# Kernel tuning notes

Measured on AMD Instinct MI355X. Metric: run time of the kernel, lower is better.

Reference implementation:

```python
import jax, jax.numpy as jnp
import numpy as np

B, H, L, DK = 8, 8, 256, 64
C = 5                 # num_clusters
DMODEL = H * DK       # 512, must equal d_k*h
U = 10 * C            # unfolding window = 50


def setup_inputs() -> dict:
    key = jax.random.key(0)
    ks = jax.random.split(key, 6)
    s = 0.05
    return {
        "K": jax.random.normal(ks[0], (B, H, L, DK), jnp.float32),
        "V": jax.random.normal(ks[1], (B, H, L, DK), jnp.float32),
        "W_k": jax.random.normal(ks[2], (DMODEL, C), jnp.float32) * s,
        "b_k": jnp.zeros((C,), jnp.float32),
        "W_q": jax.random.normal(ks[3], (DMODEL, C), jnp.float32) * s,
        "b_q": jnp.zeros((C,), jnp.float32),
        "W_back": jax.random.normal(ks[4], (C, DMODEL), jnp.float32) * s,
        "b_back": jnp.zeros((DMODEL,), jnp.float32),
    }


def _gelu(x):
    return jax.nn.gelu(x, approximate=False)  # torch default exact GELU


def reference(K, V, W_k, b_k, W_q, b_q, W_back, b_back):
    b, h, l_k, d_k = K.shape
    u = U
    num_c = W_k.shape[1]
    # torch: cat([zeros(u,h,l,d), K[1:]]) then unfold(0, u, 1) -> [b,h,l,d,u]
    padding = jnp.zeros((u, h, l_k, d_k), K.dtype)
    K_padded = jnp.concatenate([padding, K[1:]], axis=0)        # [u+b-1,h,l,d]
    idx = jnp.arange(b)[:, None] + jnp.arange(u)[None, :]        # [b,u]
    K_unf = jnp.moveaxis(K_padded[idx], 1, -1)                   # [b,h,l,d,u]
    # faithful row-major reshape, as in torch .reshape(b, l_k, -1, d_k*h)
    K_unf = K_unf.reshape(b, l_k, u, d_k * h)                    # [b,l,u,dm]

    cluster_k = jax.nn.softmax(_gelu(K_unf @ W_k + b_k), axis=-1)  # [b,l,u,C]
    cluster_q = jax.nn.softmax(_gelu(K_unf @ W_q + b_q), axis=-1)  # [b,l,u,C]

    mu = jnp.mean(cluster_q, axis=-1)                            # [b,l,u]
    sigma = jax.nn.softplus(jnp.std(cluster_q, axis=-1, ddof=1))  # unbiased std
    x = jnp.mean(cluster_k, axis=-1)
    log_prob = -0.5 * ((x - mu) / sigma) ** 2 - jnp.log(sigma) - 0.5 * jnp.log(2.0 * jnp.pi)
    # torch CrossEntropyLoss(mu, mu): input [N=b, C=l_k, d=u], soft prob targets
    ce = jnp.mean(jnp.sum(-mu * jax.nn.log_softmax(mu, axis=1), axis=1))
    loss = -jnp.mean(log_prob) + ce

    ind = jnp.argmax(cluster_q, axis=-1)                         # [b,l,u]
    # masked_fill_ zeroes positions whose argmax == i, then mean over u
    mask = ind[None] == jnp.arange(num_c)[:, None, None, None]   # [C,b,l,u]
    centers = jnp.mean(
        jnp.where(mask[..., None], 0.0, cluster_q[None]), axis=3
    )                                                            # [C,b,l,C]
    cc = _gelu(centers @ W_back + b_back)                        # [C,b,l,dm]
    cc = cc.reshape(b, h, num_c, l_k, d_k)                       # faithful reshape
    cc = jnp.max(cc, axis=2)                                     # [b,h,l,d]
    return cc, loss
```

## Files before the change

### kernel.cpp

```cpp
#include <hip/hip_runtime.h>
#include <math.h>

#define CC 5
#define NOUT 1048576

__device__ __forceinline__ float gelu_exact(float x) {
    return 0.5f * x * (1.0f + erff(x * 0.70710678118654752f));
}

__global__ __launch_bounds__(256) void cluster_main(
    const float* __restrict__ K,
    const float* __restrict__ Wk, const float* __restrict__ bk,
    const float* __restrict__ Wq, const float* __restrict__ bq,
    float* __restrict__ ws_mu, float* __restrict__ ws_lp, float* __restrict__ ws_ctr)
{
    const int tid  = threadIdx.x;
    const int wave = tid >> 6;
    const int lane = tid & 63;
    const int unit = wave * 512 + blockIdx.x;
    const int b    = unit >> 8;
    const int lp   = unit & 255;
    const int h    = lp >> 5;
    const int l0   = (lp & 31) << 3;

    __shared__ float4 WW4[512 * 3];
    __shared__ float  Ksh[4][3584];

    for (int m = tid; m < 512; m += 256) {
        const float* wkp = Wk + m * 5;
        const float* wqp = Wq + m * 5;
        WW4[m * 3 + 0] = make_float4(wkp[0], wkp[1], wkp[2], wkp[3]);
        WW4[m * 3 + 1] = make_float4(wkp[4], wqp[0], wqp[1], wqp[2]);
        WW4[m * 3 + 2] = make_float4(wqp[3], wqp[4], 0.f, 0.f);
    }
    __syncthreads();

    float* ksh = Ksh[wave];
    const int nk = b << 9;
    for (int i = lane; i < nk; i += 64) {
        int bp = i >> 9, sd = i & 511;
        ksh[sd * b + bp] = K[((((bp + 1) * 8 + h) * 256) + (l0 + (sd >> 6))) * 64 + (sd & 63)];
    }

    const int u = lane;
    if (u < 50) {
        float ak[CC], aq[CC];
        #pragma unroll
        for (int c = 0; c < CC; ++c) { ak[c] = bk[c]; aq[c] = bq[c]; }

        const int q0 = u << 9;
        const int r0 = q0 % 50;
        const int start = (50 - b) - r0;
        int B = q0 / 50;
        for (int st = start; st < 512; st += 50, ++B) {
            int jlo = st < 0 ? -st : 0;
            int jhi = min(b, 512 - st);
            const float* kp = ksh + B * b;
            for (int j = jlo; j < jhi; ++j) {
                float x = kp[j];
                int mm = (st + j) * 3;
                float4 w0 = WW4[mm], w1 = WW4[mm + 1], w2 = WW4[mm + 2];
                ak[0] = fmaf(x, w0.x, ak[0]);
                ak[1] = fmaf(x, w0.y, ak[1]);
                ak[2] = fmaf(x, w0.z, ak[2]);
                ak[3] = fmaf(x, w0.w, ak[3]);
                ak[4] = fmaf(x, w1.x, ak[4]);
                aq[0] = fmaf(x, w1.y, aq[0]);
                aq[1] = fmaf(x, w1.z, aq[1]);
                aq[2] = fmaf(x, w1.w, aq[2]);
                aq[3] = fmaf(x, w2.x, aq[3]);
                aq[4] = fmaf(x, w2.y, aq[4]);
            }
        }

        float gk[CC], gq[CC];
        float mk = -1e30f, mq = -1e30f;
        #pragma unroll
        for (int c = 0; c < CC; ++c) {
            gk[c] = gelu_exact(ak[c]); mk = fmaxf(mk, gk[c]);
            gq[c] = gelu_exact(aq[c]); mq = fmaxf(mq, gq[c]);
        }
        float sk = 0.f, sq = 0.f;
        #pragma unroll
        for (int c = 0; c < CC; ++c) {
            gk[c] = expf(gk[c] - mk); sk += gk[c];
            gq[c] = expf(gq[c] - mq); sq += gq[c];
        }
        float rsk = 1.f / sk, rsq = 1.f / sq;
        float qv[CC];
        float sumq = 0.f, sumk = 0.f;
        #pragma unroll
        for (int c = 0; c < CC; ++c) {
            float kvc = gk[c] * rsk; sumk += kvc;
            qv[c] = gq[c] * rsq;     sumq += qv[c];
        }
        float mu = sumq * 0.2f;
        float xb = sumk * 0.2f;
        float var = 0.f;
        #pragma unroll
        for (int c = 0; c < CC; ++c) { float dq = qv[c] - mu; var = fmaf(dq, dq, var); }
        var *= 0.25f;
        float sd_ = sqrtf(var);
        float sigma = log1pf(expf(sd_));
        float z = (xb - mu) / sigma;
        float logp = -0.5f * z * z - logf(sigma) - 0.91893853320467274f;
        int ind = 0; float bv = qv[0];
        #pragma unroll
        for (int c = 1; c < CC; ++c) if (qv[c] > bv) { bv = qv[c]; ind = c; }

        ws_mu[(b * 50 + u) * 256 + lp] = mu;

        float* row = ksh + u * 7;
        #pragma unroll
        for (int c = 0; c < CC; ++c) row[c] = qv[c];
        row[5] = (float)ind;
        row[6] = logp;
    }

    asm volatile("s_waitcnt lgkmcnt(0)" ::: "memory");

    const int t = lane;
    if (t < 26) {
        const float fi = (float)(t / 5);
        const int sel = (t < 25) ? (t % 5) : 6;
        const bool always = (t == 25);
        float acc = 0.f;
        for (int u2 = 0; u2 < 50; ++u2) {
            float v = ksh[u2 * 7 + sel];
            float f = ksh[u2 * 7 + 5];
            acc += (always || f != fi) ? v : 0.f;
        }
        if (t < 25) ws_ctr[unit * 25 + t] = acc * 0.02f;
        else        ws_lp[unit] = acc;
    }
}

__global__ __launch_bounds__(256) void backmap(
    const float* __restrict__ Wb, const float* __restrict__ bb,
    const float* __restrict__ ws_ctr, float* __restrict__ out)
{
    const int o = blockIdx.x * 256 + threadIdx.x;
    const int b2  = o >> 17;
    const int h2  = (o >> 14) & 7;
    const int r14 = o & 16383;
    const int m   = r14 & 511;
    const float w0 = Wb[m], w1 = Wb[512 + m], w2 = Wb[1024 + m], w3 = Wb[1536 + m], w4 = Wb[2048 + m];
    const float bias = bb[m];
    const int pbase = b2 * 655360 + h2 * 81920 + r14;
    float best = -INFINITY;
    #pragma unroll
    for (int c2 = 0; c2 < 5; ++c2) {
        int p = pbase + c2 * 16384;
        int c = p >> 20;
        int unit = (p & 1048575) >> 9;
        const float* ct = ws_ctr + unit * 25 + c * 5;
        float v = bias;
        v = fmaf(ct[0], w0, v);
        v = fmaf(ct[1], w1, v);
        v = fmaf(ct[2], w2, v);
        v = fmaf(ct[3], w3, v);
        v = fmaf(ct[4], w4, v);
        v = gelu_exact(v);
        best = fmaxf(best, v);
    }
    out[o] = best;
}

__global__ __launch_bounds__(1024) void finalize(
    const float* __restrict__ ws_mu, const float* __restrict__ ws_lp,
    float* __restrict__ out)
{
    const int tid  = threadIdx.x;
    const int wave = tid >> 6;
    const int lane = tid & 63;
    __shared__ float red[1024];
    __shared__ float total_lp_sh;
    __shared__ float cew[16];

    red[tid] = ws_lp[tid] + ws_lp[tid + 1024];
    __syncthreads();
    for (int s = 512; s > 0; s >>= 1) {
        if (tid < s) red[tid] += red[tid + s];
        __syncthreads();
    }
    if (tid == 0) total_lp_sh = red[0];

    float ce_part = 0.0f;
    for (int pair = wave; pair < 400; pair += 16) {
        const float* mp = ws_mu + pair * 256;
        float v0 = mp[lane], v1 = mp[lane + 64], v2 = mp[lane + 128], v3 = mp[lane + 192];
        float mx = fmaxf(fmaxf(v0, v1), fmaxf(v2, v3));
        #pragma unroll
        for (int off = 1; off < 64; off <<= 1) mx = fmaxf(mx, __shfl_xor(mx, off, 64));
        float se = expf(v0 - mx) + expf(v1 - mx) + expf(v2 - mx) + expf(v3 - mx);
        #pragma unroll
        for (int off = 1; off < 64; off <<= 1) se += __shfl_xor(se, off, 64);
        float lse = mx + logf(se);
        float a = -(v0 * (v0 - lse) + v1 * (v1 - lse) + v2 * (v2 - lse) + v3 * (v3 - lse));
        #pragma unroll
        for (int off = 1; off < 64; off <<= 1) a += __shfl_xor(a, off, 64);
        ce_part += a;
    }
    if (lane == 0) cew[wave] = ce_part;
    __syncthreads();
    if (tid == 0) {
        float ce = 0.0f;
        #pragma unroll
        for (int w = 0; w < 16; ++w) ce += cew[w];
        ce *= (1.0f / 400.0f);
        float loss = -(total_lp_sh * (1.0f / 102400.0f)) + ce;
        out[NOUT] = loss;
    }
}

extern "C" void kernel_launch(void* const* d_in, const int* in_sizes, int n_in,
                              void* d_out, int out_size, void* d_ws, size_t ws_size,
                              hipStream_t stream) {
    const float* K  = (const float*)d_in[0];
    const float* Wk = (const float*)d_in[2];
    const float* bk = (const float*)d_in[3];
    const float* Wq = (const float*)d_in[4];
    const float* bq = (const float*)d_in[5];
    const float* Wb = (const float*)d_in[6];
    const float* bb = (const float*)d_in[7];
    float* out    = (float*)d_out;
    float* ws_mu  = (float*)d_ws;
    float* ws_lp  = ws_mu + 102400;
    float* ws_ctr = ws_lp + 2048;

    cluster_main<<<512, 256, 0, stream>>>(K, Wk, bk, Wq, bq, ws_mu, ws_lp, ws_ctr);
    backmap<<<NOUT / 256, 256, 0, stream>>>(Wb, bb, ws_ctr, out);
    finalize<<<1, 1024, 0, stream>>>(ws_mu, ws_lp, out);
}
```

Baseline: 62.60 us.

## Split cluster dot products across 8 lanes per window and fuse backmap with finalize

cluster_main now runs one unit per 512-thread block, not one unit per wave. Each window position's reduction is split across 8 lanes by source batch, with the partial sums combined through shuffles. K is staged in block-shared memory with a padded layout. The back-projection stages the ten centre vectors in shared memory and uses GELU's shape to evaluate only at the min and max pre-activation. It is merged with the loss finalisation into one launch, which removes a kernel launch. The trade-offs are more blocks with lower per-thread work, extra block syncs, and reliance on GELU's max occurring at the argument extremes.

Measured after the change: 63.81 us. About the same (+1.9%).

```diff
diff --git a/kernel.cpp b/kernel.cpp
--- a/kernel.cpp
+++ b/kernel.cpp
@@ -8,57 +8,57 @@
     return 0.5f * x * (1.0f + erff(x * 0.70710678118654752f));
 }
 
-__global__ __launch_bounds__(256) void cluster_main(
+__global__ __launch_bounds__(512) void cluster_main(
     const float* __restrict__ K,
     const float* __restrict__ Wk, const float* __restrict__ bk,
     const float* __restrict__ Wq, const float* __restrict__ bq,
     float* __restrict__ ws_mu, float* __restrict__ ws_lp, float* __restrict__ ws_ctr)
 {
-    const int tid  = threadIdx.x;
-    const int wave = tid >> 6;
-    const int lane = tid & 63;
-    const int unit = wave * 512 + blockIdx.x;
+    const int blk  = blockIdx.x;
+    const int unit = ((blk & 7) << 8) | (blk >> 3);
     const int b    = unit >> 8;
     const int lp   = unit & 255;
     const int h    = lp >> 5;
     const int l0   = (lp & 31) << 3;
+    const int tid  = threadIdx.x;
 
     __shared__ float4 WW4[512 * 3];
-    __shared__ float  Ksh[4][3584];
-
-    for (int m = tid; m < 512; m += 256) {
-        const float* wkp = Wk + m * 5;
-        const float* wqp = Wq + m * 5;
-        WW4[m * 3 + 0] = make_float4(wkp[0], wkp[1], wkp[2], wkp[3]);
-        WW4[m * 3 + 1] = make_float4(wkp[4], wqp[0], wqp[1], wqp[2]);
-        WW4[m * 3 + 2] = make_float4(wqp[3], wqp[4], 0.f, 0.f);
-    }
-    __syncthreads();
-
-    float* ksh = Ksh[wave];
+    __shared__ float  ksh[7 * 516];
+    __shared__ float  rows[50 * 8];
+
+    {
+        const float* wkp = Wk + tid * 5;
+        const float* wqp = Wq + tid * 5;
+        WW4[tid * 3 + 0] = make_float4(wkp[0], wkp[1], wkp[2], wkp[3]);
+        WW4[tid * 3 + 1] = make_float4(wkp[4], wqp[0], wqp[1], wqp[2]);
+        WW4[tid * 3 + 2] = make_float4(wqp[3], wqp[4], 0.f, 0.f);
+    }
     const int nk = b << 9;
-    for (int i = lane; i < nk; i += 64) {
+    for (int i = tid; i < nk; i += 512) {
         int bp = i >> 9, sd = i & 511;
-        ksh[sd * b + bp] = K[((((bp + 1) * 8 + h) * 256) + (l0 + (sd >> 6))) * 64 + (sd & 63)];
-    }
-
-    const int u = lane;
-    if (u < 50) {
-        float ak[CC], aq[CC];
-        #pragma unroll
-        for (int c = 0; c < CC; ++c) { ak[c] = bk[c]; aq[c] = bq[c]; }
-
+        ksh[bp * 516 + sd] =
+            K[((((bp + 1) * 8 + h) * 256) + (l0 + (sd >> 6))) * 64 + (sd & 63)];
+    }
+    __syncthreads();
+
+    const int u = tid >> 3;
+    const int j = tid & 7;
+
+    float ak[CC] = {0.f, 0.f, 0.f, 0.f, 0.f};
+    float aq[CC] = {0.f, 0.f, 0.f, 0.f, 0.f};
+    if (u < 50 && j < b) {
+        const int usrc = 50 - b + j;
         const int q0 = u << 9;
         const int r0 = q0 % 50;
-        const int start = (50 - b) - r0;
-        int B = q0 / 50;
-        for (int st = start; st < 512; st += 50, ++B) {
-            int jlo = st < 0 ? -st : 0;
-            int jhi = min(b, 512 - st);
-            const float* kp = ksh + B * b;
-            for (int j = jlo; j < jhi; ++j) {
-                float x = kp[j];
-                int mm = (st + j) * 3;
+        int delta = usrc - r0; if (delta < 0) delta += 50;
+        int m = delta;
+        int B = (q0 + delta) / 50;
+        const float* kp = ksh + j * 516;
+        #pragma unroll
+        for (int it = 0; it < 11; ++it) {
+            if (m < 512) {
+                float x = kp[B];
+                int mm = m * 3;
                 float4 w0 = WW4[mm], w1 = WW4[mm + 1], w2 = WW4[mm + 2];
                 ak[0] = fmaf(x, w0.x, ak[0]);
                 ak[1] = fmaf(x, w0.y, ak[1]);
@@ -71,14 +71,25 @@
                 aq[3] = fmaf(x, w2.x, aq[3]);
                 aq[4] = fmaf(x, w2.y, aq[4]);
             }
-        }
-
+            m += 50; ++B;
+        }
+    }
+    #pragma unroll
+    for (int off = 4; off; off >>= 1) {
+        #pragma unroll
+        for (int c = 0; c < CC; ++c) {
+            ak[c] += __shfl_down(ak[c], off, 8);
+            aq[c] += __shfl_down(aq[c], off, 8);
+        }
+    }
+
+    if (u < 50 && j == 0) {
         float gk[CC], gq[CC];
         float mk = -1e30f, mq = -1e30f;
         #pragma unroll
         for (int c = 0; c < CC; ++c) {
-            gk[c] = gelu_exact(ak[c]); mk = fmaxf(mk, gk[c]);
-            gq[c] = gelu_exact(aq[c]); mq = fmaxf(mq, gq[c]);
+            gk[c] = gelu_exact(ak[c] + bk[c]); mk = fmaxf(mk, gk[c]);
+            gq[c] = gelu_exact(aq[c] + bq[c]); mq = fmaxf(mq, gq[c]);
         }
         float sk = 0.f, sq = 0.f;
         #pragma unroll
@@ -109,68 +120,73 @@
         for (int c = 1; c < CC; ++c) if (qv[c] > bv) { bv = qv[c]; ind = c; }
 
         ws_mu[(b * 50 + u) * 256 + lp] = mu;
-
-        float* row = ksh + u * 7;
+        float* row = rows + u * 8;
         #pragma unroll
         for (int c = 0; c < CC; ++c) row[c] = qv[c];
         row[5] = (float)ind;
         row[6] = logp;
     }
-
-    asm volatile("s_waitcnt lgkmcnt(0)" ::: "memory");
-
-    const int t = lane;
-    if (t < 26) {
-        const float fi = (float)(t / 5);
-        const int sel = (t < 25) ? (t % 5) : 6;
-        const bool always = (t == 25);
+    __syncthreads();
+
+    if (tid < 26) {
+        const float fi = (float)(tid / 5);
+        const int sel = (tid < 25) ? (tid % 5) : 6;
+        const bool always = (tid == 25);
         float acc = 0.f;
         for (int u2 = 0; u2 < 50; ++u2) {
-            float v = ksh[u2 * 7 + sel];
-            float f = ksh[u2 * 7 + 5];
+            float v = rows[u2 * 8 + sel];
+            float f = rows[u2 * 8 + 5];
             acc += (always || f != fi) ? v : 0.f;
         }
-        if (t < 25) ws_ctr[unit * 25 + t] = acc * 0.02f;
-        else        ws_lp[unit] = acc;
-    }
-}
-
-__global__ __launch_bounds__(256) void backmap(
+        if (tid < 25) ws_ctr[unit * 25 + tid] = acc * 0.02f;
+        else          ws_lp[unit] = acc;
+    }
+}
+
+__global__ __launch_bounds__(1024) void backfin(
     const float* __restrict__ Wb, const float* __restrict__ bb,
-    const float* __restrict__ ws_ctr, float* __restrict__ out)
+    const float* __restrict__ ws_ctr, const float* __restrict__ ws_mu,
+    const float* __restrict__ ws_lp, float* __restrict__ out)
 {
-    const int o = blockIdx.x * 256 + threadIdx.x;
-    const int b2  = o >> 17;
-    const int h2  = (o >> 14) & 7;
-    const int r14 = o & 16383;
-    const int m   = r14 & 511;
-    const float w0 = Wb[m], w1 = Wb[512 + m], w2 = Wb[1024 + m], w3 = Wb[1536 + m], w4 = Wb[2048 + m];
-    const float bias = bb[m];
-    const int pbase = b2 * 655360 + h2 * 81920 + r14;
-    float best = -INFINITY;
-    #pragma unroll
-    for (int c2 = 0; c2 < 5; ++c2) {
-        int p = pbase + c2 * 16384;
-        int c = p >> 20;
-        int unit = (p & 1048575) >> 9;
-        const float* ct = ws_ctr + unit * 25 + c * 5;
-        float v = bias;
-        v = fmaf(ct[0], w0, v);
-        v = fmaf(ct[1], w1, v);
-        v = fmaf(ct[2], w2, v);
-        v = fmaf(ct[3], w3, v);
-        v = fmaf(ct[4], w4, v);
-        v = gelu_exact(v);
-        best = fmaxf(best, v);
-    }
-    out[o] = best;
-}
-
-__global__ __launch_bounds__(1024) void finalize(
-    const float* __restrict__ ws_mu, const float* __restrict__ ws_lp,
-    float* __restrict__ out)
-{
-    const int tid  = threadIdx.x;
+    const int tid = threadIdx.x;
+
+    if (blockIdx.x < 1024) {
+        __shared__ float ct[10][5];
+        const int o0 = blockIdx.x << 10;
+        const int b2 = o0 >> 17;
+        const int h2 = (o0 >> 14) & 7;
+        const int r0 = o0 & 16383;
+        if (tid < 50) {
+            int c2 = tid / 10, hf = (tid / 5) & 1, k = tid % 5;
+            int p = b2 * 655360 + h2 * 81920 + r0 + c2 * 16384 + hf * 512;
+            int c = p >> 20;
+            int un = (p >> 9) & 2047;
+            ct[c2 * 2 + hf][k] = ws_ctr[un * 25 + c * 5 + k];
+        }
+        __syncthreads();
+
+        const int m  = tid & 511;
+        const int hf = tid >> 9;
+        const float w0 = Wb[m], w1 = Wb[512 + m], w2 = Wb[1024 + m],
+                    w3 = Wb[1536 + m], w4 = Wb[2048 + m];
+        const float bias = bb[m];
+        float zmin = INFINITY, zmax = -INFINITY;
+        #pragma unroll
+        for (int c2 = 0; c2 < 5; ++c2) {
+            const float* c5 = ct[c2 * 2 + hf];
+            float z = bias;
+            z = fmaf(c5[0], w0, z);
+            z = fmaf(c5[1], w1, z);
+            z = fmaf(c5[2], w2, z);
+            z = fmaf(c5[3], w3, z);
+            z = fmaf(c5[4], w4, z);
+            zmin = fminf(zmin, z);
+            zmax = fmaxf(zmax, z);
+        }
+        out[o0 + tid] = fmaxf(gelu_exact(zmin), gelu_exact(zmax));
+        return;
+    }
+
     const int wave = tid >> 6;
     const int lane = tid & 63;
     __shared__ float red[1024];
@@ -228,7 +244,6 @@
     float* ws_lp  = ws_mu + 102400;
     float* ws_ctr = ws_lp + 2048;
 
-    cluster_main<<<512, 256, 0, stream>>>(K, Wk, bk, Wq, bq, ws_mu, ws_lp, ws_ctr);
-    backmap<<<NOUT / 256, 256, 0, stream>>>(Wb, bb, ws_ctr, out);
-    finalize<<<1, 1024, 0, stream>>>(ws_mu, ws_lp, out);
-}
+    cluster_main<<<2048, 512, 0, stream>>>(K, Wk, bk, Wq, bq, ws_mu, ws_lp, ws_ctr);
+    backfin<<<1025, 1024, 0, stream>>>(Wb, bb, ws_ctr, ws_mu, ws_lp, out);
+}
```
